# Kernel tuning notes

Measured on AMD Instinct MI355X. Metric: run time of the kernel, lower is better.

Reference implementation:

```python
import jax, jax.numpy as jnp
import numpy as np

B, C, O, H, W = 4, 64, 64, 128, 128
KH = KW = 3
K = KH * KW  # 9 kernel positions
MRM = 10.0   # max_residue_magnitude


def setup_inputs() -> dict:
    key = jax.random.key(0)
    ks = jax.random.split(key, 6)
    return {
        "x_main": jax.random.normal(ks[0], (B, C, H, W), jnp.float32),
        "x_extra": jax.random.normal(ks[1], (B, C, H, W), jnp.float32),
        "pre_offset": jax.random.normal(ks[2], (B, K, H, W, 2), jnp.float32) * 2.0,
        "pre_sim": jax.random.uniform(ks[3], (B, K, H, W), jnp.float32),
        "weight": jax.random.normal(ks[4], (O, C, KH, KW), jnp.float32) / np.sqrt(C * K),
        "bias": jnp.zeros((O,), jnp.float32),
        "w_om": jax.random.normal(ks[5], (3 * K, C, KH, KW), jnp.float32) * 0.01,
        "b_om": jnp.zeros((3 * K,), jnp.float32),
    }


def _bilinear(img, py, px):
    """img: [C,Hi,Wi]; py, px: [K,Ho,Wo] float sample coords. Zero padding outside."""
    Hi, Wi = img.shape[1], img.shape[2]
    y0 = jnp.floor(py)
    x0 = jnp.floor(px)
    dy = py - y0  # [K,Ho,Wo]
    dx = px - x0

    def gather(yi, xi):
        valid = ((yi >= 0) & (yi <= Hi - 1) & (xi >= 0) & (xi <= Wi - 1)).astype(img.dtype)
        yc = jnp.clip(yi, 0, Hi - 1).astype(jnp.int32)
        xc = jnp.clip(xi, 0, Wi - 1).astype(jnp.int32)
        return img[:, yc, xc] * valid[None]  # [C,K,Ho,Wo]

    v00 = gather(y0, x0)
    v01 = gather(y0, x0 + 1)
    v10 = gather(y0 + 1, x0)
    v11 = gather(y0 + 1, x0 + 1)
    return (v00 * (1 - dy) * (1 - dx) + v01 * (1 - dy) * dx
            + v10 * dy * (1 - dx) + v11 * dy * dx)


def reference(x_main, x_extra, pre_offset, pre_sim, weight, bias, w_om, b_om):
    # conv_offset_mask: 3x3, stride 1, pad 1 -> [B, 3K, H, W]
    out = jax.lax.conv_general_dilated(
        x_extra, w_om, (1, 1), ((1, 1), (1, 1)),
        dimension_numbers=("NCHW", "OIHW", "NCHW")) + b_om[None, :, None, None]
    o1, o2, mask = jnp.split(out, 3, axis=1)  # each [B,K,H,W]
    offset = MRM * jnp.tanh(jnp.concatenate([o1, o2], axis=1))  # [B,2K,H,W]
    # pre_offset reorder: even channels <- pre_offset[...,1] (y), odd <- pre_offset[...,0] (x)
    off_y = offset[:, 0::2] + pre_offset[..., 1]  # [B,K,H,W]
    off_x = offset[:, 1::2] + pre_offset[..., 0]
    mask = jax.nn.sigmoid(mask * pre_sim)  # use_sim=True

    f32 = offset.dtype
    ky = (jnp.arange(K) // KW).astype(f32)  # kernel row per position k
    kx = (jnp.arange(K) % KW).astype(f32)   # kernel col per position k
    # base grid: p = out_pos*stride - pad + k*dil = h - 1 + ky (stride=1,pad=1,dil=1)
    py = off_y + (jnp.arange(H, dtype=f32)[None, None, :, None] - 1.0) + ky[None, :, None, None]
    px = off_x + (jnp.arange(W, dtype=f32)[None, None, None, :] - 1.0) + kx[None, :, None, None]

    sampled = jax.vmap(_bilinear)(x_main, py, px)      # [B,C,K,H,W]
    sampled = sampled * mask[:, None]                   # modulated (DCNv2)
    y = jnp.einsum("bckhw,ock->bohw", sampled, weight.reshape(O, C, K))
    return y + bias[None, :, None, None]
```

## Files before the change

### kernel.cpp

```cpp
#include <hip/hip_runtime.h>
#include <math.h>

#define Bn 4
#define Cn 64
#define On 64
#define Hn 128
#define Wn 128
#define Kn 9
#define HWn (Hn*Wn)
#define ZROW 16384
#define XBSTRIDE (16385*64)

typedef _Float16 v8h __attribute__((ext_vector_type(8)));
typedef _Float16 v2h __attribute__((ext_vector_type(2)));
typedef float v4f __attribute__((ext_vector_type(4)));

__device__ inline unsigned short f2h(float f) {
  _Float16 h = (_Float16)f;
  return __builtin_bit_cast(unsigned short, h);
}
__device__ inline _Float16 u2h(unsigned v) {
  return __builtin_bit_cast(_Float16, (unsigned short)(v & 0xffff));
}
__device__ inline v8h sp8(_Float16 x) { v8h v = {x,x,x,x,x,x,x,x}; return v; }

__global__ __launch_bounds__(256) void k_prep(
    const float* __restrict__ x_main,
    const float* __restrict__ x_extra,
    const float* __restrict__ weight,
    const float* __restrict__ w_om,
    _Float16* __restrict__ xT,
    _Float16* __restrict__ xeF,
    _Float16* __restrict__ Wfrag,
    _Float16* __restrict__ WOMfrag)
{
  const int blk = blockIdx.x;
  const int t = threadIdx.x;

  if (blk < 2048) {
    __shared__ float tile[64 * 65];
    int isExtra = blk >> 10;
    int b  = (blk >> 8) & 3;
    int p0 = (blk & 255) << 6;
    const float* src = (isExtra ? x_extra : x_main) + b * Cn * HWn + p0;
    #pragma unroll
    for (int i = 0; i < 4; ++i) {
      int c  = i * 16 + (t >> 4);
      int p4 = (t & 15) * 4;
      float4 v = *(const float4*)(src + c * HWn + p4);
      tile[c * 65 + p4 + 0] = v.x;
      tile[c * 65 + p4 + 1] = v.y;
      tile[c * 65 + p4 + 2] = v.z;
      tile[c * 65 + p4 + 3] = v.w;
    }
    __syncthreads();
    _Float16* dst = (isExtra ? xeF : xT) + b * XBSTRIDE + p0 * 64;
    #pragma unroll
    for (int i = 0; i < 8; ++i) {
      int p  = i * 8 + (t >> 5);
      int c2 = (t & 31) * 2;
      v2h pk = { (_Float16)tile[c2 * 65 + p], (_Float16)tile[(c2 + 1) * 65 + p] };
      *(v2h*)(dst + p * 64 + c2) = pk;
    }
  } else {
    int rb = blk - 2048;
    for (int idx = rb * 256 + t; idx < 36864; idx += 64 * 256) {
      int j  = idx & 7;
      int ln = (idx >> 3) & 63;
      int ot = (idx >> 9) & 3;
      int hk = (idx >> 11) & 1;
      int k  = idx >> 12;
      int o = ot * 16 + (ln & 15);
      int c = hk * 32 + (ln >> 4) * 8 + j;
      Wfrag[idx] = (_Float16)weight[(o * Cn + c) * Kn + k];
    }
    for (int idx = rb * 256 + t; idx < 18432; idx += 64 * 256) {
      int j    = idx & 7;
      int ln   = (idx >> 3) & 63;
      int jt   = (idx >> 9) & 1;
      int half = (idx >> 10) & 1;
      int k9   = idx >> 11;
      int jo = jt * 16 + (ln & 15);
      int c  = half * 32 + (ln >> 4) * 8 + j;
      float v = (jo < 27) ? w_om[(jo * Cn + c) * Kn + k9] : 0.f;
      WOMfrag[idx] = (_Float16)v;
    }
    if (rb == 0 && t < 256) {
      int b = t >> 6, c = t & 63;
      xT[b * XBSTRIDE + ZROW * 64 + c] = (_Float16)0.f;
      xeF[b * XBSTRIDE + ZROW * 64 + c] = (_Float16)0.f;
    }
  }
}

__global__ __launch_bounds__(256, 4) void k_fused(
    const _Float16* __restrict__ xT,
    const _Float16* __restrict__ xeF,
    const _Float16* __restrict__ Wfrag,
    const _Float16* __restrict__ WOMfrag,
    const float* __restrict__ pre_offset,
    const float* __restrict__ pre_sim,
    const float* __restrict__ b_om,
    const float* __restrict__ bias,
    float* __restrict__ out)
{
  __shared__ float jbuf[4 * 16 * 36];
  __shared__ uint4 recbuf[4 * 16 * 9];
  __shared__ __align__(16) _Float16 Abuf[2][8 * 512];

  const int t    = threadIdx.x;
  const int lane = t & 63;
  const int wv   = __builtin_amdgcn_readfirstlane(t >> 6);
  const int raw  = blockIdx.x;
  const int blk  = ((raw & 7) << 7) | (raw >> 3);
  const int b    = blk >> 8;
  const int h    = (blk >> 1) & 127;
  const int wq   = (blk & 1) * 4 + wv;
  const int kq   = lane >> 4;
  const int n    = lane & 15;
  const int w    = wq * 16 + n;

  unsigned tapoff[9];
  #pragma unroll
  for (int k9 = 0; k9 < 9; ++k9) {
    int r  = h - 1 + k9 / 3;
    int cc = w - 1 + k9 % 3;
    bool v = ((unsigned)r < (unsigned)Hn) & ((unsigned)cc < (unsigned)Wn);
    tapoff[k9] = (v ? (unsigned)(r * Wn + cc) : (unsigned)ZROW) * 64u;
  }

  const _Float16* xe = xeF + b * XBSTRIDE;
  const v8h* Wom = (const v8h*)WOMfrag;
  v4f ca0 = {0,0,0,0}, ca1 = {0,0,0,0};
  for (int k9 = 0; k9 < 9; ++k9) {
    #pragma unroll
    for (int half = 0; half < 2; ++half) {
      int abase = ((k9 * 2 + half) * 2) * 64 + lane;
      v8h A0 = Wom[abase];
      v8h A1 = Wom[abase + 64];
      v8h Bt = *(const v8h*)(xe + tapoff[k9] + half * 32 + kq * 8);
      ca0 = __builtin_amdgcn_mfma_f32_16x16x32_f16(A0, Bt, ca0, 0, 0, 0);
      ca1 = __builtin_amdgcn_mfma_f32_16x16x32_f16(A1, Bt, ca1, 0, 0, 0);
    }
  }

  float* jb = jbuf + wv * (16 * 36);
  *(v4f*)(jb + n * 36 + kq * 4)      = ca0;
  *(v4f*)(jb + n * 36 + 16 + kq * 4) = ca1;

  uint4* rb = recbuf + wv * (16 * 9);
  if (kq < 3) {
    #pragma unroll
    for (int kk = 0; kk < 3; ++kk) {
      int k = kq * 3 + kk;
      float sy = jb[n * 36 + 2 * k]     + b_om[2 * k];
      float sx = jb[n * 36 + 2 * k + 1] + b_om[2 * k + 1];
      float sm = jb[n * 36 + 18 + k]    + b_om[18 + k];
      int pbase = ((b * Kn + k) * Hn + h) * Wn + w;
      float2 po = *(const float2*)(pre_offset + pbase * 2);
      float ey = __expf(2.f * sy);
      float ex = __expf(2.f * sx);
      float py = 10.f - 20.f / (ey + 1.f) + po.y + (float)(h - 1 + k / 3);
      float px = 10.f - 20.f / (ex + 1.f) + po.x + (float)(w - 1 + k % 3);
      float m  = 1.f / (1.f + __expf(-sm * pre_sim[pbase]));
      float fy = floorf(py), fx = floorf(px);
      float dy = py - fy, dx = px - fx;
      int y0 = (int)fy, x0 = (int)fx;
      int y1 = y0 + 1, x1 = x0 + 1;
      bool vy0 = (y0 >= 0) & (y0 < Hn), vy1 = (y1 >= 0) & (y1 < Hn);
      bool vx0 = (x0 >= 0) & (x0 < Wn), vx1 = (x1 >= 0) & (x1 < Wn);
      unsigned r00 = (vy0 & vx0) ? (unsigned)(y0 * Wn + x0) : ZROW;
      unsigned r01 = (vy0 & vx1) ? (unsigned)(y0 * Wn + x1) : ZROW;
      unsigned r10 = (vy1 & vx0) ? (unsigned)(y1 * Wn + x0) : ZROW;
      unsigned r11 = (vy1 & vx1) ? (unsigned)(y1 * Wn + x1) : ZROW;
      float wy0 = 1.f - dy, wx0 = 1.f - dx;
      uint4 rec;
      rec.x = r00 | (r01 << 16);
      rec.y = r10 | (r11 << 16);
      rec.z = (unsigned)f2h(wy0 * wx0 * m) | ((unsigned)f2h(wy0 * dx * m) << 16);
      rec.w = (unsigned)f2h(dy * wx0 * m) | ((unsigned)f2h(dy * dx * m) << 16);
      rb[n * 9 + k] = rec;
    }
  }

  v4f acc0 = {0,0,0,0}, acc1 = {0,0,0,0}, acc2 = {0,0,0,0}, acc3 = {0,0,0,0};
  const _Float16* xb = xT + b * XBSTRIDE;
  const v8h* Wf = (const v8h*)Wfrag;

  if (wv == 0) {
    #pragma unroll
    for (int f = 0; f < 8; ++f) {
      v8h g = Wf[(0 * 8 + f) * 64 + lane];
      *(v8h*)(&Abuf[0][f * 512 + lane * 8]) = g;
    }
  }
  __syncthreads();

  uint4 rec0   = rb[n * 9 + 0];
  uint4 rec_nx = rb[n * 9 + 1];
  _Float16 h00 = u2h(rec0.z), h01 = u2h(rec0.z >> 16);
  _Float16 h10 = u2h(rec0.w), h11 = u2h(rec0.w >> 16);
  unsigned o00 = (rec0.x & 0xffff) * 64u + kq * 8;
  unsigned o01 = (rec0.x >> 16)    * 64u + kq * 8;
  unsigned o10 = (rec0.y & 0xffff) * 64u + kq * 8;
  unsigned o11 = (rec0.y >> 16)    * 64u + kq * 8;
  v8h C0 = *(const v8h*)(xb + o00);
  v8h C1 = *(const v8h*)(xb + o01);
  v8h C2 = *(const v8h*)(xb + o10);
  v8h C3 = *(const v8h*)(xb + o11);

  #pragma unroll
  for (int k = 0; k < 9; ++k) {
    if (k < 8 && wv == ((k + 1) & 3)) {
      #pragma unroll
      for (int f = 0; f < 8; ++f) {
        v8h g = Wf[((k + 1) * 8 + f) * 64 + lane];
        *(v8h*)(&Abuf[(k + 1) & 1][f * 512 + lane * 8]) = g;
      }
    }
    v8h H0 = *(const v8h*)(xb + o00 + 32);
    v8h H1 = *(const v8h*)(xb + o01 + 32);
    v8h H2 = *(const v8h*)(xb + o10 + 32);
    v8h H3 = *(const v8h*)(xb + o11 + 32);

    v8h N0, N1, N2, N3;
    _Float16 nh00 = (_Float16)0.f, nh01 = (_Float16)0.f;
    _Float16 nh10 = (_Float16)0.f, nh11 = (_Float16)0.f;
    unsigned p00 = 0, p01 = 0, p10 = 0, p11 = 0;
    if (k < 8) {
      nh00 = u2h(rec_nx.z); nh01 = u2h(rec_nx.z >> 16);
      nh10 = u2h(rec_nx.w); nh11 = u2h(rec_nx.w >> 16);
      p00 = (rec_nx.x & 0xffff) * 64u + kq * 8;
      p01 = (rec_nx.x >> 16)    * 64u + kq * 8;
      p10 = (rec_nx.y & 0xffff) * 64u + kq * 8;
      p11 = (rec_nx.y >> 16)    * 64u + kq * 8;
      N0 = *(const v8h*)(xb + p00);
      N1 = *(const v8h*)(xb + p01);
      N2 = *(const v8h*)(xb + p10);
      N3 = *(const v8h*)(xb + p11);
    }
    uint4 rec_nx2 = rec_nx;
    if (k < 7) rec_nx2 = rb[n * 9 + k + 2];

    __builtin_amdgcn_sched_barrier(0);

    const v8h* Ab = (const v8h*)Abuf[k & 1];
    v8h F0 = Ab[0 * 64 + lane], F1 = Ab[1 * 64 + lane];
    v8h F2 = Ab[2 * 64 + lane], F3 = Ab[3 * 64 + lane];

    v8h Bf0 = C0 * sp8(h00) + C1 * sp8(h01) + C2 * sp8(h10) + C3 * sp8(h11);

    acc0 = __builtin_amdgcn_mfma_f32_16x16x32_f16(F0, Bf0, acc0, 0, 0, 0);
    acc1 = __builtin_amdgcn_mfma_f32_16x16x32_f16(F1, Bf0, acc1, 0, 0, 0);
    acc2 = __builtin_amdgcn_mfma_f32_16x16x32_f16(F2, Bf0, acc2, 0, 0, 0);
    acc3 = __builtin_amdgcn_mfma_f32_16x16x32_f16(F3, Bf0, acc3, 0, 0, 0);

    v8h F4 = Ab[4 * 64 + lane], F5 = Ab[5 * 64 + lane];
    v8h F6 = Ab[6 * 64 + lane], F7 = Ab[7 * 64 + lane];
    v8h Bf1 = H0 * sp8(h00) + H1 * sp8(h01) + H2 * sp8(h10) + H3 * sp8(h11);

    acc0 = __builtin_amdgcn_mfma_f32_16x16x32_f16(F4, Bf1, acc0, 0, 0, 0);
    acc1 = __builtin_amdgcn_mfma_f32_16x16x32_f16(F5, Bf1, acc1, 0, 0, 0);
    acc2 = __builtin_amdgcn_mfma_f32_16x16x32_f16(F6, Bf1, acc2, 0, 0, 0);
    acc3 = __builtin_amdgcn_mfma_f32_16x16x32_f16(F7, Bf1, acc3, 0, 0, 0);

    if (k < 8) {
      C0 = N0; C1 = N1; C2 = N2; C3 = N3;
      h00 = nh00; h01 = nh01; h10 = nh10; h11 = nh11;
      o00 = p00; o01 = p01; o10 = p10; o11 = p11;
      rec_nx = rec_nx2;
    }

    if (k < 8) {
      asm volatile("s_waitcnt lgkmcnt(0)" ::: "memory");
      __builtin_amdgcn_s_barrier();
    }
  }

  const float4* b4 = (const float4*)bias;
  float4 vb0 = b4[0 * 4 + kq], vb1 = b4[1 * 4 + kq];
  float4 vb2 = b4[2 * 4 + kq], vb3 = b4[3 * 4 + kq];
  float* ob = out + (b * On) * HWn + h * Wn + wq * 16 + n;
  #pragma unroll
  for (int reg = 0; reg < 4; ++reg) {
    ob[(0 * 16 + kq * 4 + reg) * HWn] = acc0[reg] + ((const float*)&vb0)[reg];
    ob[(1 * 16 + kq * 4 + reg) * HWn] = acc1[reg] + ((const float*)&vb1)[reg];
    ob[(2 * 16 + kq * 4 + reg) * HWn] = acc2[reg] + ((const float*)&vb2)[reg];
    ob[(3 * 16 + kq * 4 + reg) * HWn] = acc3[reg] + ((const float*)&vb3)[reg];
  }
}

extern "C" void kernel_launch(void* const* d_in, const int* in_sizes, int n_in,
                              void* d_out, int out_size, void* d_ws, size_t ws_size,
                              hipStream_t stream) {
  const float* x_main     = (const float*)d_in[0];
  const float* x_extra    = (const float*)d_in[1];
  const float* pre_offset = (const float*)d_in[2];
  const float* pre_sim    = (const float*)d_in[3];
  const float* weight     = (const float*)d_in[4];
  const float* bias       = (const float*)d_in[5];
  const float* w_om       = (const float*)d_in[6];
  const float* b_om       = (const float*)d_in[7];
  float* out = (float*)d_out;

  char* ws = (char*)d_ws;
  _Float16* xT      = (_Float16*)(ws);
  _Float16* xeF     = (_Float16*)(ws + 8389120);
  _Float16* Wfrag   = (_Float16*)(ws + 16778240);
  _Float16* WOMfrag = (_Float16*)(ws + 16851968);

  k_prep<<<2112, 256, 0, stream>>>(x_main, x_extra, weight, w_om,
                                   xT, xeF, Wfrag, WOMfrag);
  k_fused<<<1024, 256, 0, stream>>>(xT, xeF, Wfrag, WOMfrag,
                                    pre_offset, pre_sim, b_om, bias, out);
}
```

Before: 145.0 us.

## Stage weight fragments via direct global-to-LDS loads and double-buffer offset conv

Replaces the register round-trip weight staging with global_load_lds direct-to-LDS copies in both the main modulated conv loop and the offset/mask conv. The offset conv now double-buffers its weight fragments in LDS and prefetches the next tap's activations, with vmcnt-based waits and barriers. The prep kernel's transpose also writes 16-byte packed fp16 vectors instead of 4-byte pairs. The aim is to cut register pressure and VGPR-to-LDS traffic and to overlap loads with MFMA work. In exchange it relies on fragile vmcnt counting, where a wrong count could race on LDS.

```diff
diff --git a/kernel.cpp b/kernel.cpp
--- a/kernel.cpp
+++ b/kernel.cpp
@@ -23,6 +23,12 @@
   return __builtin_bit_cast(_Float16, (unsigned short)(v & 0xffff));
 }
 __device__ inline v8h sp8(_Float16 x) { v8h v = {x,x,x,x,x,x,x,x}; return v; }
+
+__device__ inline void gld_lds16(const void* g, void* s) {
+  __builtin_amdgcn_global_load_lds(
+      (const __attribute__((address_space(1))) unsigned int*)g,
+      (__attribute__((address_space(3))) unsigned int*)s, 16, 0, 0);
+}
 
 __global__ __launch_bounds__(256) void k_prep(
     const float* __restrict__ x_main,
@@ -55,12 +61,16 @@
     }
     __syncthreads();
     _Float16* dst = (isExtra ? xeF : xT) + b * XBSTRIDE + p0 * 64;
-    #pragma unroll
-    for (int i = 0; i < 8; ++i) {
-      int p  = i * 8 + (t >> 5);
-      int c2 = (t & 31) * 2;
-      v2h pk = { (_Float16)tile[c2 * 65 + p], (_Float16)tile[(c2 + 1) * 65 + p] };
-      *(v2h*)(dst + p * 64 + c2) = pk;
+    int q  = t & 7;
+    int pr = t >> 3;
+    #pragma unroll
+    for (int i = 0; i < 2; ++i) {
+      int p = i * 32 + pr;
+      v8h pk;
+      #pragma unroll
+      for (int j = 0; j < 8; ++j)
+        pk[j] = (_Float16)tile[(q * 8 + j) * 65 + p];
+      *(v8h*)(dst + p * 64 + q * 8) = pk;
     }
   } else {
     int rb = blk - 2048;
@@ -132,21 +142,60 @@
   const _Float16* xe = xeF + b * XBSTRIDE;
   const v8h* Wom = (const v8h*)WOMfrag;
   v4f ca0 = {0,0,0,0}, ca1 = {0,0,0,0};
+
+  if (wv == 0) {
+    #pragma unroll
+    for (int f = 0; f < 4; ++f)
+      gld_lds16(Wom + (0 * 4 + f) * 64 + lane, &Abuf[0][f * 512]);
+  }
+  __builtin_amdgcn_sched_barrier(0);
+  v8h Bt0 = *(const v8h*)(xe + tapoff[0] + kq * 8);
+  v8h Bt1 = *(const v8h*)(xe + tapoff[0] + 32 + kq * 8);
+  asm volatile("s_waitcnt vmcnt(2)" ::: "memory");
+  __builtin_amdgcn_s_barrier();
+
+  #pragma unroll
   for (int k9 = 0; k9 < 9; ++k9) {
-    #pragma unroll
-    for (int half = 0; half < 2; ++half) {
-      int abase = ((k9 * 2 + half) * 2) * 64 + lane;
-      v8h A0 = Wom[abase];
-      v8h A1 = Wom[abase + 64];
-      v8h Bt = *(const v8h*)(xe + tapoff[k9] + half * 32 + kq * 8);
-      ca0 = __builtin_amdgcn_mfma_f32_16x16x32_f16(A0, Bt, ca0, 0, 0, 0);
-      ca1 = __builtin_amdgcn_mfma_f32_16x16x32_f16(A1, Bt, ca1, 0, 0, 0);
+    if (k9 < 8 && wv == ((k9 + 1) & 3)) {
+      #pragma unroll
+      for (int f = 0; f < 4; ++f)
+        gld_lds16(Wom + ((k9 + 1) * 4 + f) * 64 + lane,
+                  &Abuf[(k9 + 1) & 1][f * 512]);
+    }
+    __builtin_amdgcn_sched_barrier(0);
+    v8h Bn0, Bn1;
+    if (k9 < 8) {
+      Bn0 = *(const v8h*)(xe + tapoff[k9 + 1] + kq * 8);
+      Bn1 = *(const v8h*)(xe + tapoff[k9 + 1] + 32 + kq * 8);
+    }
+    __builtin_amdgcn_sched_barrier(0);
+    const v8h* Sb = (const v8h*)Abuf[k9 & 1];
+    v8h A00 = Sb[0 * 64 + lane], A01 = Sb[1 * 64 + lane];
+    ca0 = __builtin_amdgcn_mfma_f32_16x16x32_f16(A00, Bt0, ca0, 0, 0, 0);
+    ca1 = __builtin_amdgcn_mfma_f32_16x16x32_f16(A01, Bt0, ca1, 0, 0, 0);
+    v8h A10 = Sb[2 * 64 + lane], A11 = Sb[3 * 64 + lane];
+    ca0 = __builtin_amdgcn_mfma_f32_16x16x32_f16(A10, Bt1, ca0, 0, 0, 0);
+    ca1 = __builtin_amdgcn_mfma_f32_16x16x32_f16(A11, Bt1, ca1, 0, 0, 0);
+    if (k9 < 8) {
+      Bt0 = Bn0; Bt1 = Bn1;
+      asm volatile("s_waitcnt vmcnt(2)" ::: "memory");
+      __builtin_amdgcn_s_barrier();
     }
   }
 
   float* jb = jbuf + wv * (16 * 36);
   *(v4f*)(jb + n * 36 + kq * 4)      = ca0;
   *(v4f*)(jb + n * 36 + 16 + kq * 4) = ca1;
+
+  __builtin_amdgcn_s_barrier();
+
+  const v8h* Wf = (const v8h*)Wfrag;
+  if (wv == 0) {
+    #pragma unroll
+    for (int f = 0; f < 8; ++f)
+      gld_lds16(Wf + (0 * 8 + f) * 64 + lane, &Abuf[0][f * 512]);
+  }
+  __builtin_amdgcn_sched_barrier(0);
 
   uint4* rb = recbuf + wv * (16 * 9);
   if (kq < 3) {
@@ -185,16 +234,6 @@
 
   v4f acc0 = {0,0,0,0}, acc1 = {0,0,0,0}, acc2 = {0,0,0,0}, acc3 = {0,0,0,0};
   const _Float16* xb = xT + b * XBSTRIDE;
-  const v8h* Wf = (const v8h*)Wfrag;
-
-  if (wv == 0) {
-    #pragma unroll
-    for (int f = 0; f < 8; ++f) {
-      v8h g = Wf[(0 * 8 + f) * 64 + lane];
-      *(v8h*)(&Abuf[0][f * 512 + lane * 8]) = g;
-    }
-  }
-  __syncthreads();
 
   uint4 rec0   = rb[n * 9 + 0];
   uint4 rec_nx = rb[n * 9 + 1];
@@ -208,16 +247,18 @@
   v8h C1 = *(const v8h*)(xb + o01);
   v8h C2 = *(const v8h*)(xb + o10);
   v8h C3 = *(const v8h*)(xb + o11);
+  asm volatile("s_waitcnt vmcnt(4)" ::: "memory");
+  __builtin_amdgcn_s_barrier();
 
   #pragma unroll
   for (int k = 0; k < 9; ++k) {
     if (k < 8 && wv == ((k + 1) & 3)) {
       #pragma unroll
-      for (int f = 0; f < 8; ++f) {
-        v8h g = Wf[((k + 1) * 8 + f) * 64 + lane];
-        *(v8h*)(&Abuf[(k + 1) & 1][f * 512 + lane * 8]) = g;
-      }
-    }
+      for (int f = 0; f < 8; ++f)
+        gld_lds16(Wf + ((k + 1) * 8 + f) * 64 + lane,
+                  &Abuf[(k + 1) & 1][f * 512]);
+    }
+    __builtin_amdgcn_sched_barrier(0);
     v8h H0 = *(const v8h*)(xb + o00 + 32);
     v8h H1 = *(const v8h*)(xb + o01 + 32);
     v8h H2 = *(const v8h*)(xb + o10 + 32);
@@ -269,10 +310,7 @@
       h00 = nh00; h01 = nh01; h10 = nh10; h11 = nh11;
       o00 = p00; o01 = p01; o10 = p10; o11 = p11;
       rec_nx = rec_nx2;
-    }
-
-    if (k < 8) {
-      asm volatile("s_waitcnt lgkmcnt(0)" ::: "memory");
+      asm volatile("s_waitcnt vmcnt(4)" ::: "memory");
       __builtin_amdgcn_s_barrier();
     }
   }
```

After: 143.1 us. About the same (-1.3%).
